# Kernel optimization log

Measured on AMD Instinct MI355X. Metric: run time of the kernel, lower is better.

Reference implementation:

```python
import jax, jax.numpy as jnp
import numpy as np

N = 100000      # nodes
E = 625000      # edges
F_IN = 128      # num_features
C = 32          # num_classes


def setup_inputs() -> dict:
    key = jax.random.key(0)
    k1, k2, k3, k4, k5 = jax.random.split(key, 5)
    x = jax.random.normal(k1, (N, F_IN), dtype=jnp.float32)
    edge_index = jax.random.randint(k2, (2, E), 0, N, dtype=jnp.int64)
    s = 1.0 / np.sqrt(F_IN)
    # PyG SAGEConv: lin_l (applied to aggregated neighbors, with bias), lin_r (applied to self, no bias)
    W_l = jax.random.uniform(k3, (C, F_IN), dtype=jnp.float32, minval=-s, maxval=s)
    b_l = jax.random.uniform(k4, (C,), dtype=jnp.float32, minval=-s, maxval=s)
    W_r = jax.random.uniform(k5, (C, F_IN), dtype=jnp.float32, minval=-s, maxval=s)
    return {"x": x, "edge_index": edge_index, "W_l": W_l, "b_l": b_l, "W_r": W_r}


def reference(x, edge_index, W_l, b_l, W_r):
    src, dst = edge_index[0], edge_index[1]
    # mean aggregation of source-node features at destination nodes
    msg_sum = jax.ops.segment_sum(x[src], dst, num_segments=N)            # [N, F]
    deg = jax.ops.segment_sum(jnp.ones((E,), x.dtype), dst, num_segments=N)
    agg = msg_sum / jnp.maximum(deg, 1.0)[:, None]
    # SAGEConv: lin_l(agg) + lin_r(x)
    h = agg @ W_l.T + b_l + x @ W_r.T                                     # [N, C]
    h = jax.nn.relu(h)
    # dropout is identity in eval mode
    return jax.nn.log_softmax(h, axis=1)
```

## Files before the change

### kernel.cpp

```cpp
#include <hip/hip_runtime.h>
#include <hip/hip_fp16.h>
#include <math.h>

#define F_IN 128
#define NCLS 32
#define ZC   64
#define CAP  64
#define NPART 8
#define PADW 136

typedef __attribute__((ext_vector_type(8))) short short8v;
typedef __attribute__((ext_vector_type(4))) float f32x4;

__device__ __forceinline__ unsigned int pk2(float lo, float hi) {
    unsigned int a = __float_as_uint(lo), b = __float_as_uint(hi);
    a = (a + 0x7fffu + ((a >> 16) & 1u)) >> 16;
    b = (b + 0x7fffu + ((b >> 16) & 1u)) >> 16;
    return a | (b << 16);
}
__device__ __forceinline__ uint4 pack8(float4 a, float4 b) {
    return make_uint4(pk2(a.x, a.y), pk2(a.z, a.w), pk2(b.x, b.y), pk2(b.z, b.w));
}

__global__ __launch_bounds__(256) void zero_kernel(int* __restrict__ cnt, int N) {
    int i = blockIdx.x * 256 + threadIdx.x;
    if (i < N) cnt[i] = 0;
}

__device__ __forceinline__ void dev_fill_unit(const void* __restrict__ ei, int is64,
                                              int* __restrict__ cnt, int* __restrict__ col,
                                              int E, int N, int span, int u, int t) {
    int part = u & (NPART - 1);
    int e0 = ((u >> 3) * 256 + t) * 4;
    if (e0 >= E) return;
    int lo = part * span;
    int hi = lo + span; if (hi > N) hi = N;
    int ecnt = (E - e0 >= 4) ? 4 : (E - e0);

    int d[4];
    if (is64) {
        const long long* dp = (const long long*)ei + E + e0;
        if (ecnt == 4) {
            longlong2 d01 = *(const longlong2*)dp, d23 = *(const longlong2*)(dp + 2);
            d[0]=(int)d01.x; d[1]=(int)d01.y; d[2]=(int)d23.x; d[3]=(int)d23.y;
        } else {
            for (int j = 0; j < ecnt; ++j) d[j] = (int)dp[j];
        }
    } else {
        const int* dp = (const int*)ei + E + e0;
        if (ecnt == 4) {
            int4 dv = *(const int4*)dp;
            d[0]=dv.x; d[1]=dv.y; d[2]=dv.z; d[3]=dv.w;
        } else {
            for (int j = 0; j < ecnt; ++j) d[j] = dp[j];
        }
    }

    for (int j = 0; j < ecnt; ++j) {
        if (d[j] >= lo && d[j] < hi) {
            int sv = is64 ? (int)((const long long*)ei)[e0 + j]
                          : ((const int*)ei)[e0 + j];
            if ((unsigned)sv >= (unsigned)N) sv = 0;
            int pos = atomicAdd(&cnt[d[j]], 1);
            if (pos < CAP) col[(size_t)d[j] * CAP + pos] = sv;
        }
    }
}

__global__ __launch_bounds__(256) void projfill_kernel(const float* __restrict__ x,
                                                       const void* __restrict__ ei,
                                                       const float* __restrict__ Wl,
                                                       const float* __restrict__ Wr,
                                                       __half* __restrict__ z,
                                                       int* __restrict__ cnt,
                                                       int* __restrict__ col,
                                                       int N, int E, int span, int FU) {
    __shared__ __align__(16) unsigned short xs[64 * PADW];
    __shared__ __align__(16) unsigned short ws[64 * PADW];
    int t = threadIdx.x;
    int b = blockIdx.x;

    if (b < FU) {
        const unsigned int* u32 = (const unsigned int*)ei;
        unsigned int aa = 0;
        #pragma unroll
        for (int j = 0; j < 16; ++j) aa |= u32[2 * j + 1];
        int is64 = (aa == 0u);
        dev_fill_unit(ei, is64, cnt, col, E, N, span, b, t);
        return;
    }

    int node0 = (b - FU) * 64;

    #pragma unroll
    for (int p = 0; p < 4; ++p) {
        int idx = t + p * 256;
        int row = idx >> 4;
        int q   = idx & 15;
        const float* srcW = (row < NCLS) ? (Wl + row * F_IN) : (Wr + (row - NCLS) * F_IN);
        float4 wa = *(const float4*)(srcW + q * 8);
        float4 wb = *(const float4*)(srcW + q * 8 + 4);
        *(uint4*)(ws + row * PADW + q * 8) = pack8(wa, wb);

        int node = node0 + row;
        int safe = (node < N) ? node : (N - 1);
        const float* srcX = x + (size_t)safe * F_IN;
        float4 xa = *(const float4*)(srcX + q * 8);
        float4 xb = *(const float4*)(srcX + q * 8 + 4);
        *(uint4*)(xs + row * PADW + q * 8) = pack8(xa, xb);
    }
    __syncthreads();

    int wave = t >> 6;
    int lane = t & 63;
    int l15  = lane & 15;
    int koff = (lane >> 4) * 8;

    f32x4 acc[4] = {{0.f,0.f,0.f,0.f},{0.f,0.f,0.f,0.f},{0.f,0.f,0.f,0.f},{0.f,0.f,0.f,0.f}};
    const unsigned short* xrow = xs + (wave * 16 + l15) * PADW + koff;
    const unsigned short* wrow = ws + l15 * PADW + koff;

    #pragma unroll
    for (int ks = 0; ks < 4; ++ks) {
        short8v a = *reinterpret_cast<const short8v*>(xrow + ks * 32);
        #pragma unroll
        for (int ct = 0; ct < 4; ++ct) {
            short8v bfr = *reinterpret_cast<const short8v*>(wrow + ct * 16 * PADW + ks * 32);
            acc[ct] = __builtin_amdgcn_mfma_f32_16x16x32_bf16(a, bfr, acc[ct], 0, 0, 0);
        }
    }

    int r0 = (lane >> 4) * 4;
    #pragma unroll
    for (int ct = 0; ct < 4; ++ct) {
        #pragma unroll
        for (int r = 0; r < 4; ++r) {
            int node = node0 + wave * 16 + r0 + r;
            if (node < N) z[(size_t)node * ZC + ct * 16 + l15] = __float2half(acc[ct][r]);
        }
    }
}

__global__ __launch_bounds__(256) void finish_kernel(const __half* __restrict__ z,
                                                     const int* __restrict__ col,
                                                     const int* __restrict__ cnt,
                                                     const float* __restrict__ bl,
                                                     float* __restrict__ out, int N) {
    int gid = blockIdx.x * 256 + threadIdx.x;
    int node = gid >> 5;
    int c = gid & 31;
    if (node >= N) return;

    int deg = cnt[node];
    int m = (deg < CAP) ? deg : CAP;
    const int* cb = col + (size_t)node * CAP;
    float selfz = __half2float(z[(size_t)node * ZC + NCLS + c]);
    float bias  = bl[c];

    float a[8] = {};
    for (int base = 0; base < m; base += 8) {
        int4 n0 = *(const int4*)(cb + base);
        int4 n1 = *(const int4*)(cb + base + 4);
        int idx[8] = {n0.x, n0.y, n0.z, n0.w, n1.x, n1.y, n1.z, n1.w};
        #pragma unroll
        for (int k = 0; k < 8; ++k) {
            bool ok = (base + k < m);
            int s = ok ? idx[k] : 0;
            float v = __half2float(z[(size_t)s * ZC + c]);
            a[k] += ok ? v : 0.f;
        }
    }
    float acc = ((a[0] + a[1]) + (a[2] + a[3])) + ((a[4] + a[5]) + (a[6] + a[7]));

    float inv = 1.0f / fmaxf((float)deg, 1.0f);
    float h = acc * inv + bias + selfz;
    h = fmaxf(h, 0.f);

    float mx = h;
    #pragma unroll
    for (int o = 16; o >= 1; o >>= 1) mx = fmaxf(mx, __shfl_xor(mx, o));
    float p = h - mx;
    float ex = __expf(p);
    float s = ex;
    #pragma unroll
    for (int o = 16; o >= 1; o >>= 1) s += __shfl_xor(s, o);

    out[(size_t)node * NCLS + c] = p - __logf(s);
}

__global__ void detect_i64_kernel(const unsigned int* __restrict__ ei, int* __restrict__ flag) {
    if (blockIdx.x == 0 && threadIdx.x == 0) {
        unsigned int acc = 0;
        #pragma unroll
        for (int i = 0; i < 64; ++i) acc |= ei[2 * i + 1];
        *flag = (acc == 0u) ? 1 : 0;
    }
}

__global__ __launch_bounds__(256) void scatter_kernel(const float* __restrict__ x,
                                                      const void* __restrict__ ei,
                                                      const int* __restrict__ flag,
                                                      float* __restrict__ msg,
                                                      float* __restrict__ deg, int E, int N) {
    long long gid = (long long)blockIdx.x * blockDim.x + threadIdx.x;
    int e = (int)(gid >> 5);
    if (e >= E) return;
    int c = (int)(gid & 31);
    int is64 = *flag;
    int src = is64 ? (int)((const long long*)ei)[e] : ((const int*)ei)[e];
    int dst = is64 ? (int)((const long long*)ei)[(size_t)E + e] : ((const int*)ei)[(size_t)E + e];
    if ((unsigned)src >= (unsigned)N || (unsigned)dst >= (unsigned)N) return;
    float4 v = *(const float4*)(x + (size_t)src * F_IN + (c << 2));
    float* m = msg + (size_t)dst * F_IN + (c << 2);
    atomicAdd(m + 0, v.x);
    atomicAdd(m + 1, v.y);
    atomicAdd(m + 2, v.z);
    atomicAdd(m + 3, v.w);
    if (c == 0) atomicAdd(deg + dst, 1.0f);
}

__global__ __launch_bounds__(256) void apply_kernel(const float* __restrict__ x,
                                                    const float* __restrict__ msg,
                                                    const float* __restrict__ degf,
                                                    const float* __restrict__ Wl,
                                                    const float* __restrict__ bl,
                                                    const float* __restrict__ Wr,
                                                    float* __restrict__ out, int N) {
    int n = blockIdx.x * 256 + threadIdx.x;
    if (n >= N) return;
    float inv = 1.0f / fmaxf(degf[n], 1.0f);
    float acc[NCLS];
    #pragma unroll
    for (int c = 0; c < NCLS; ++c) acc[c] = bl[c];
    const float* xr = x + (size_t)n * F_IN;
    const float* mr = msg + (size_t)n * F_IN;
    for (int kb = 0; kb < F_IN; kb += 4) {
        float4 xv = *(const float4*)(xr + kb);
        float4 mv = *(const float4*)(mr + kb);
        float b0 = mv.x * inv, b1 = mv.y * inv, b2 = mv.z * inv, b3 = mv.w * inv;
        #pragma unroll
        for (int c = 0; c < NCLS; ++c) {
            float4 wl = *(const float4*)(Wl + c * F_IN + kb);
            float4 wr = *(const float4*)(Wr + c * F_IN + kb);
            acc[c] += b0 * wl.x + b1 * wl.y + b2 * wl.z + b3 * wl.w
                    + xv.x * wr.x + xv.y * wr.y + xv.z * wr.z + xv.w * wr.w;
        }
    }
    float mx = 0.0f;
    #pragma unroll
    for (int c = 0; c < NCLS; ++c) { acc[c] = fmaxf(acc[c], 0.0f); mx = fmaxf(mx, acc[c]); }
    float s = 0.0f;
    #pragma unroll
    for (int c = 0; c < NCLS; ++c) s += __expf(acc[c] - mx);
    float lg = __logf(s);
    float* o = out + (size_t)n * NCLS;
    #pragma unroll
    for (int q = 0; q < NCLS; q += 4) {
        float4 w = make_float4(acc[q] - mx - lg, acc[q + 1] - mx - lg,
                               acc[q + 2] - mx - lg, acc[q + 3] - mx - lg);
        *(float4*)(o + q) = w;
    }
}

extern "C" void kernel_launch(void* const* d_in, const int* in_sizes, int n_in,
                              void* d_out, int out_size, void* d_ws, size_t ws_size,
                              hipStream_t stream) {
    const float* x  = (const float*)d_in[0];
    const void*  ei = d_in[1];
    const float* Wl = (const float*)d_in[2];
    const float* bl = (const float*)d_in[3];
    const float* Wr = (const float*)d_in[4];

    int N = in_sizes[0] / F_IN;
    int E = in_sizes[1] / 2;
    int span = (N + NPART - 1) / NPART;

    size_t need = (size_t)N * ZC * 2 + (size_t)N * 4 + (size_t)N * CAP * 4;

    if (ws_size >= need) {
        __half* z   = (__half*)d_ws;
        int*    cnt = (int*)((char*)d_ws + (size_t)N * ZC * 2);
        int*    col = cnt + N;
        float*  outp = (float*)d_out;

        int T  = (N + 63) / 64;
        int FU = ((E + 1023) / 1024) * NPART;

        zero_kernel<<<(N + 255) / 256, 256, 0, stream>>>(cnt, N);
        projfill_kernel<<<FU + T, 256, 0, stream>>>(x, ei, Wl, Wr, z, cnt, col,
                                                    N, E, span, FU);
        long long tot = (long long)N * 32;
        finish_kernel<<<(int)((tot + 255) / 256), 256, 0, stream>>>(z, col, cnt, bl,
                                                                    outp, N);
    } else {
        float* msg  = (float*)d_ws;
        float* deg  = msg + (size_t)N * F_IN;
        int*   flag = (int*)(deg + N);

        hipMemsetAsync(d_ws, 0, ((size_t)N * F_IN + N) * 4, stream);
        detect_i64_kernel<<<1, 64, 0, stream>>>((const unsigned int*)ei, flag);

        long long tot = (long long)E * 32;
        scatter_kernel<<<(int)((tot + 255) / 256), 256, 0, stream>>>(x, ei, flag, msg, deg, E, N);
        apply_kernel<<<(N + 255) / 256, 256, 0, stream>>>(x, msg, deg, Wl, bl, Wr,
                                                          (float*)d_out, N);
    }
}
```

Before: 68.67 us.

## Split fused projection/fill kernel and pre-pack weights to bf16 once

The combined projection+CSR-fill kernel is split into separate proj and fill launches. The weights are packed to bf16 once in the init kernel instead of in every block. The projection now loads x straight from global memory into MFMA registers without LDS staging or a barrier. This removes the per-block weight conversion and the LDS round trip, and raises occupancy. In exchange the fill and projection work no longer overlap within one launch, and there is an extra kernel launch.

```diff
diff --git a/kernel.cpp b/kernel.cpp
--- a/kernel.cpp
+++ b/kernel.cpp
@@ -7,7 +7,7 @@
 #define ZC   64
 #define CAP  64
 #define NPART 8
-#define PADW 136
+#define WROWS 64
 
 typedef __attribute__((ext_vector_type(8))) short short8v;
 typedef __attribute__((ext_vector_type(4))) float f32x4;
@@ -22,16 +22,80 @@
     return make_uint4(pk2(a.x, a.y), pk2(a.z, a.w), pk2(b.x, b.y), pk2(b.z, b.w));
 }
 
-__global__ __launch_bounds__(256) void zero_kernel(int* __restrict__ cnt, int N) {
-    int i = blockIdx.x * 256 + threadIdx.x;
+__global__ __launch_bounds__(256) void init_kernel(const float* __restrict__ Wl,
+                                                   const float* __restrict__ Wr,
+                                                   unsigned short* __restrict__ wb,
+                                                   int* __restrict__ cnt, int N) {
+    int t = threadIdx.x;
+    int i = blockIdx.x * 256 + t;
     if (i < N) cnt[i] = 0;
-}
-
-__device__ __forceinline__ void dev_fill_unit(const void* __restrict__ ei, int is64,
-                                              int* __restrict__ cnt, int* __restrict__ col,
-                                              int E, int N, int span, int u, int t) {
-    int part = u & (NPART - 1);
-    int e0 = ((u >> 3) * 256 + t) * 4;
+    if (blockIdx.x == 0) {
+        #pragma unroll
+        for (int p = 0; p < 4; ++p) {
+            int idx = t + p * 256;
+            int row = idx >> 4;
+            int q   = idx & 15;
+            const float* srcW = (row < NCLS) ? (Wl + row * F_IN) : (Wr + (row - NCLS) * F_IN);
+            float4 a = *(const float4*)(srcW + q * 8);
+            float4 b = *(const float4*)(srcW + q * 8 + 4);
+            *(uint4*)(wb + row * F_IN + q * 8) = pack8(a, b);
+        }
+    }
+}
+
+__global__ __launch_bounds__(256) void proj_kernel(const float* __restrict__ x,
+                                                   const unsigned short* __restrict__ wb,
+                                                   __half* __restrict__ z, int N) {
+    int t = threadIdx.x;
+    int node0 = blockIdx.x * 64;
+    int wave = t >> 6;
+    int lane = t & 63;
+    int l15  = lane & 15;
+    int koff = (lane >> 4) * 8;
+
+    int row  = node0 + wave * 16 + l15;
+    int safe = (row < N) ? row : (N - 1);
+    const float* xr = x + (size_t)safe * F_IN + koff;
+    const unsigned short* wr = wb + l15 * F_IN + koff;
+
+    f32x4 acc[4] = {{0.f,0.f,0.f,0.f},{0.f,0.f,0.f,0.f},{0.f,0.f,0.f,0.f},{0.f,0.f,0.f,0.f}};
+
+    #pragma unroll
+    for (int ks = 0; ks < 4; ++ks) {
+        float4 xa = *(const float4*)(xr + ks * 32);
+        float4 xb = *(const float4*)(xr + ks * 32 + 4);
+        uint4 ap = pack8(xa, xb);
+        short8v a = *reinterpret_cast<short8v*>(&ap);
+        #pragma unroll
+        for (int ct = 0; ct < 4; ++ct) {
+            short8v b = *reinterpret_cast<const short8v*>(wr + ct * 16 * F_IN + ks * 32);
+            acc[ct] = __builtin_amdgcn_mfma_f32_16x16x32_bf16(a, b, acc[ct], 0, 0, 0);
+        }
+    }
+
+    int r0 = (lane >> 4) * 4;
+    #pragma unroll
+    for (int ct = 0; ct < 4; ++ct) {
+        #pragma unroll
+        for (int r = 0; r < 4; ++r) {
+            int node = node0 + wave * 16 + r0 + r;
+            if (node < N) z[(size_t)node * ZC + ct * 16 + l15] = __float2half(acc[ct][r]);
+        }
+    }
+}
+
+__global__ __launch_bounds__(256) void fill_kernel(const void* __restrict__ ei,
+                                                   int* __restrict__ cnt,
+                                                   int* __restrict__ col,
+                                                   int E, int N, int span) {
+    const unsigned int* u32 = (const unsigned int*)ei;
+    unsigned int aa = 0;
+    #pragma unroll
+    for (int j = 0; j < 16; ++j) aa |= u32[2 * j + 1];
+    int is64 = (aa == 0u);
+
+    int part = blockIdx.x & (NPART - 1);
+    int e0 = ((blockIdx.x >> 3) * 256 + threadIdx.x) * 4;
     if (e0 >= E) return;
     int lo = part * span;
     int hi = lo + span; if (hi > N) hi = N;
@@ -63,80 +127,6 @@
             if ((unsigned)sv >= (unsigned)N) sv = 0;
             int pos = atomicAdd(&cnt[d[j]], 1);
             if (pos < CAP) col[(size_t)d[j] * CAP + pos] = sv;
-        }
-    }
-}
-
-__global__ __launch_bounds__(256) void projfill_kernel(const float* __restrict__ x,
-                                                       const void* __restrict__ ei,
-                                                       const float* __restrict__ Wl,
-                                                       const float* __restrict__ Wr,
-                                                       __half* __restrict__ z,
-                                                       int* __restrict__ cnt,
-                                                       int* __restrict__ col,
-                                                       int N, int E, int span, int FU) {
-    __shared__ __align__(16) unsigned short xs[64 * PADW];
-    __shared__ __align__(16) unsigned short ws[64 * PADW];
-    int t = threadIdx.x;
-    int b = blockIdx.x;
-
-    if (b < FU) {
-        const unsigned int* u32 = (const unsigned int*)ei;
-        unsigned int aa = 0;
-        #pragma unroll
-        for (int j = 0; j < 16; ++j) aa |= u32[2 * j + 1];
-        int is64 = (aa == 0u);
-        dev_fill_unit(ei, is64, cnt, col, E, N, span, b, t);
-        return;
-    }
-
-    int node0 = (b - FU) * 64;
-
-    #pragma unroll
-    for (int p = 0; p < 4; ++p) {
-        int idx = t + p * 256;
-        int row = idx >> 4;
-        int q   = idx & 15;
-        const float* srcW = (row < NCLS) ? (Wl + row * F_IN) : (Wr + (row - NCLS) * F_IN);
-        float4 wa = *(const float4*)(srcW + q * 8);
-        float4 wb = *(const float4*)(srcW + q * 8 + 4);
-        *(uint4*)(ws + row * PADW + q * 8) = pack8(wa, wb);
-
-        int node = node0 + row;
-        int safe = (node < N) ? node : (N - 1);
-        const float* srcX = x + (size_t)safe * F_IN;
-        float4 xa = *(const float4*)(srcX + q * 8);
-        float4 xb = *(const float4*)(srcX + q * 8 + 4);
-        *(uint4*)(xs + row * PADW + q * 8) = pack8(xa, xb);
-    }
-    __syncthreads();
-
-    int wave = t >> 6;
-    int lane = t & 63;
-    int l15  = lane & 15;
-    int koff = (lane >> 4) * 8;
-
-    f32x4 acc[4] = {{0.f,0.f,0.f,0.f},{0.f,0.f,0.f,0.f},{0.f,0.f,0.f,0.f},{0.f,0.f,0.f,0.f}};
-    const unsigned short* xrow = xs + (wave * 16 + l15) * PADW + koff;
-    const unsigned short* wrow = ws + l15 * PADW + koff;
-
-    #pragma unroll
-    for (int ks = 0; ks < 4; ++ks) {
-        short8v a = *reinterpret_cast<const short8v*>(xrow + ks * 32);
-        #pragma unroll
-        for (int ct = 0; ct < 4; ++ct) {
-            short8v bfr = *reinterpret_cast<const short8v*>(wrow + ct * 16 * PADW + ks * 32);
-            acc[ct] = __builtin_amdgcn_mfma_f32_16x16x32_bf16(a, bfr, acc[ct], 0, 0, 0);
-        }
-    }
-
-    int r0 = (lane >> 4) * 4;
-    #pragma unroll
-    for (int ct = 0; ct < 4; ++ct) {
-        #pragma unroll
-        for (int r = 0; r < 4; ++r) {
-            int node = node0 + wave * 16 + r0 + r;
-            if (node < N) z[(size_t)node * ZC + ct * 16 + l15] = __float2half(acc[ct][r]);
         }
     }
 }
@@ -275,20 +265,22 @@
     int E = in_sizes[1] / 2;
     int span = (N + NPART - 1) / NPART;
 
-    size_t need = (size_t)N * ZC * 2 + (size_t)N * 4 + (size_t)N * CAP * 4;
+    size_t need = (size_t)N * ZC * 2 + (size_t)N * 4 + (size_t)N * CAP * 4
+                + (size_t)WROWS * F_IN * 2;
 
     if (ws_size >= need) {
         __half* z   = (__half*)d_ws;
         int*    cnt = (int*)((char*)d_ws + (size_t)N * ZC * 2);
         int*    col = cnt + N;
+        unsigned short* wb = (unsigned short*)(col + (size_t)N * CAP);
         float*  outp = (float*)d_out;
 
         int T  = (N + 63) / 64;
         int FU = ((E + 1023) / 1024) * NPART;
 
-        zero_kernel<<<(N + 255) / 256, 256, 0, stream>>>(cnt, N);
-        projfill_kernel<<<FU + T, 256, 0, stream>>>(x, ei, Wl, Wr, z, cnt, col,
-                                                    N, E, span, FU);
+        init_kernel<<<(N + 255) / 256, 256, 0, stream>>>(Wl, Wr, wb, cnt, N);
+        proj_kernel<<<T, 256, 0, stream>>>(x, wb, z, N);
+        fill_kernel<<<FU, 256, 0, stream>>>(ei, cnt, col, E, N, span);
         long long tot = (long long)N * 32;
         finish_kernel<<<(int)((tot + 255) / 256), 256, 0, stream>>>(z, col, cnt, bl,
                                                                     outp, N);
```

Result: slower. 83.65 us (+21.8%).
